# Kernel tuning notes

Measured on AMD Instinct MI355X. Metric: run time of the kernel, lower is better.

Reference implementation:

```python
import jax, jax.numpy as jnp
import numpy as np

B, IN_SIZE, IN_DIM = 16, 2048, 512
HEADS, OUT_SIZE = 4, 64
EPS = 0.1
MAX_ITER = 30
SIGMA = 0.1


def setup_inputs() -> dict:
    key = jax.random.key(0)
    k1, k2 = jax.random.split(key)
    x = jax.random.normal(k1, (B, IN_SIZE, IN_DIM), dtype=jnp.float32)
    stdv = 1.0 / np.sqrt(OUT_SIZE)
    weight = jax.random.uniform(k2, (HEADS, OUT_SIZE, IN_DIM), jnp.float32, -stdv, stdv)
    return {"x": x, "weight": weight}


def _position_filter(in_size, out_size, sigma):
    # 1-D gaussian position filter (image=False branch of get_position_filter)
    a = jnp.arange(0.0, in_size, dtype=jnp.float32)[:, None] / in_size
    b = jnp.arange(0.0, out_size, dtype=jnp.float32)[None, :] / out_size
    return jnp.exp(-(((a - b) / sigma) ** 2))  # (in_size, out_size)


def log_sinkhorn(K, iterations):
    """Log-domain Sinkhorn. K: (B, H, N, M) log-kernel.
    Row marginal a = 1/N (uniform, no mask). Scaling vectors are
    detached (envelope trick) before forming the transport plan,
    matching the original OTK implementation."""
    Bn, H, N, M = K.shape
    log_a = jnp.full((Bn, H, N), -jnp.log(jnp.float32(N)), dtype=K.dtype)
    u0 = jnp.zeros((Bn, H, N), K.dtype)
    v0 = jnp.zeros((Bn, H, M), K.dtype)

    def step(carry, _):
        u, v = carry
        Z = K + u[..., :, None] + v[..., None, :]
        u = log_a - jax.nn.logsumexp(Z, axis=-1)
        Z = K + u[..., :, None] + v[..., None, :]
        v = -jax.nn.logsumexp(Z, axis=-2)
        return (u, v), None

    (u, v), _ = jax.lax.scan(step, (u0, v0), None, length=iterations)
    u = jax.lax.stop_gradient(u)
    v = jax.lax.stop_gradient(v)
    return jnp.exp(K + u[..., :, None] + v[..., None, :])  # (B,H,N,M)


def reference(x, weight):
    # x: (B, N, D); weight: (H, M, D)
    pf = _position_filter(IN_SIZE, OUT_SIZE, SIGMA)  # (N, M)
    # euclidean cost via expansion (cdist)
    x2 = jnp.sum(x * x, axis=-1)                      # (B, N)
    w2 = jnp.sum(weight * weight, axis=-1)            # (H, M)
    xw = jnp.einsum('bnd,hmd->bhnm', x, weight)       # (B, H, N, M)
    C = jnp.sqrt(jnp.maximum(x2[:, None, :, None] + w2[None, :, None, :] - 2.0 * xw, 0.0))
    K = (-C / EPS) * pf[None, None]                   # position filter applied to log-kernel
    P = log_sinkhorn(K, MAX_ITER)                     # (B, H, N, M) transport plan
    # attn: (B, M, H, N) -> (B, M*H, N)
    attn = jnp.transpose(P, (0, 3, 1, 2)).reshape(B, OUT_SIZE * HEADS, IN_SIZE)
    out = jnp.matmul(attn, x)                         # (B, M*H, D)
    return out.reshape(B, OUT_SIZE, HEADS * IN_DIM)
```

## Files before the change

kernel.cpp:

```cpp
#include <hip/hip_runtime.h>
#include <hip/hip_fp16.h>


typedef _Float16 h2 __attribute__((ext_vector_type(2)));
typedef _Float16 h8 __attribute__((ext_vector_type(8)));
typedef float f4 __attribute__((ext_vector_type(4)));

#define NB 16
#define NN 2048
#define ND 512
#define NH 4
#define NM 64
#define NITER 30
#define EUSCALE 8.0f

static __device__ __forceinline__ float fdot2f(h2 a, h2 b, float c) {
#if __has_builtin(__builtin_amdgcn_fdot2)
  return __builtin_amdgcn_fdot2(a, b, c, false);
#else
  return (float)a[0] * (float)b[0] + (float)a[1] * (float)b[1] + c;
#endif
}

static __device__ __forceinline__ h2 pkrtz(float a, float b) {
  return __builtin_bit_cast(h2, __builtin_amdgcn_cvt_pkrtz(a, b));
}

static __device__ __forceinline__ h8 pack8(float4 a, float4 b) {
  h8 r;
  r[0] = (_Float16)a.x; r[1] = (_Float16)a.y; r[2] = (_Float16)a.z; r[3] = (_Float16)a.w;
  r[4] = (_Float16)b.x; r[5] = (_Float16)b.y; r[6] = (_Float16)b.z; r[7] = (_Float16)b.w;
  return r;
}

static __device__ __forceinline__ float sq4(float4 a) {
  return a.x * a.x + a.y * a.y + a.z * a.z + a.w * a.w;
}

__global__ __launch_bounds__(512) void k01_fused(const float* __restrict__ x,
                                                 const float* __restrict__ w,
                                                 _Float16* __restrict__ xT,
                                                 _Float16* __restrict__ E) {
  extern __shared__ __align__(16) char smem[];
  const int bid = blockIdx.x;
  const int tid = threadIdx.x;

  if (bid < 2048) {
    auto tile = (float(*)[65])smem;
    const int sub = tid >> 8;
    const int t = tid & 255;
    const int xt = bid & 15;
    const int dt = (bid >> 4) & 7;
    const int b = bid >> 7;
    const int n0 = (xt * 2 + sub) * 64;
    const int d0 = dt * 64;
    const int rbase = sub << 6;

    const int nr = t >> 2;
    const int ds = (t & 3) * 16;
    const float4* src = (const float4*)(x + ((size_t)(b * NN + n0 + nr) * ND + d0 + ds));
    float4 v0 = src[0], v1 = src[1], v2 = src[2], v3 = src[3];
    float vals[16] = {v0.x, v0.y, v0.z, v0.w, v1.x, v1.y, v1.z, v1.w,
                      v2.x, v2.y, v2.z, v2.w, v3.x, v3.y, v3.z, v3.w};
#pragma unroll
    for (int j = 0; j < 16; ++j) tile[rbase + ds + j][nr] = vals[j];
    __syncthreads();
    const int dr = t >> 2;
    const int ns = (t & 3) * 16;
    h8 o0, o1;
#pragma unroll
    for (int j = 0; j < 8; ++j) o0[j] = (_Float16)tile[rbase + dr][ns + j];
#pragma unroll
    for (int j = 0; j < 8; ++j) o1[j] = (_Float16)tile[rbase + dr][ns + 8 + j];
    _Float16* dst = xT + ((size_t)(b * ND + d0 + dr) * NN + n0 + ns);
    *(h8*)dst = o0;
    *(h8*)(dst + 8) = o1;
    return;
  }

  auto Ah  = (_Float16(*)[72])(smem);
  auto Bh  = (_Float16(*)[72])(smem + 18432);
  auto x2s = (float(*)[4])(smem + 55296);
  auto w2s = (float(*)[2])(smem + 57344);
  float* x2r = (float*)(smem + 59392);
  float* w2r = (float*)(smem + 59904);

  const int bid2 = bid - 2048;
  const int b = bid2 >> 4;
  const int n0 = (bid2 & 15) * 128;
  const int lane = tid & 63;
  const int wv = tid >> 6;
  const int lrow = lane & 15;
  const int kq = lane >> 4;

  f4 acc[16];
#pragma unroll
  for (int i = 0; i < 16; ++i) acc[i] = (f4){0.f, 0.f, 0.f, 0.f};

  const int ar = tid >> 2, ac = (tid & 3) * 16;
  const int br = tid >> 1, bc = (tid & 1) * 32;
  const float* xsrc = x + ((size_t)(b * NN + n0 + ar) * ND + ac);
  const float* wsrc = w + ((size_t)br * ND + bc);
  float x2p = 0.f, w2p = 0.f;

  for (int kt = 0; kt < 8; ++kt) {
    {
      const float4* s4 = (const float4*)(xsrc + kt * 64);
      float4 a0 = s4[0], a1 = s4[1], a2 = s4[2], a3 = s4[3];
      x2p += sq4(a0) + sq4(a1) + sq4(a2) + sq4(a3);
      *(h8*)&Ah[ar][ac] = pack8(a0, a1);
      *(h8*)&Ah[ar][ac + 8] = pack8(a2, a3);
    }
    {
      const float4* s4 = (const float4*)(wsrc + kt * 64);
      float4 u0 = s4[0], u1 = s4[1], u2 = s4[2], u3 = s4[3];
      float4 u4 = s4[4], u5 = s4[5], u6 = s4[6], u7 = s4[7];
      w2p += sq4(u0) + sq4(u1) + sq4(u2) + sq4(u3)
           + sq4(u4) + sq4(u5) + sq4(u6) + sq4(u7);
      *(h8*)&Bh[br][bc] = pack8(u0, u1);
      *(h8*)&Bh[br][bc + 8] = pack8(u2, u3);
      *(h8*)&Bh[br][bc + 16] = pack8(u4, u5);
      *(h8*)&Bh[br][bc + 24] = pack8(u6, u7);
    }
    __syncthreads();
#pragma unroll
    for (int s = 0; s < 2; ++s) {
      h8 af = *(const h8*)&Ah[wv * 16 + lrow][s * 32 + kq * 8];
#pragma unroll
      for (int cf = 0; cf < 16; ++cf) {
        h8 bf = *(const h8*)&Bh[cf * 16 + lrow][s * 32 + kq * 8];
        acc[cf] = __builtin_amdgcn_mfma_f32_16x16x32_f16(af, bf, acc[cf], 0, 0, 0);
      }
    }
    __syncthreads();
  }

  x2s[ar][tid & 3] = x2p;
  w2s[br][tid & 1] = w2p;
  __syncthreads();
  if (tid < 128) {
    x2r[tid] = x2s[tid][0] + x2s[tid][1] + x2s[tid][2] + x2s[tid][3];
  } else if (tid < 384) {
    const int r = tid - 128;
    w2r[r] = w2s[r][0] + w2s[r][1];
  }
  __syncthreads();

#pragma unroll
  for (int cf = 0; cf < 16; ++cf) {
    const int mg = cf * 16 + lrow;
    const int hh = mg >> 6;
    const int m = mg & 63;
    const float w2v = w2r[mg];
    const float bm = (float)m * (1.0f / 64.0f);
    _Float16* Eb = E + ((size_t)(b * NH + hh) * NN) * NM;
#pragma unroll
    for (int j = 0; j < 4; ++j) {
      const int nl = wv * 16 + kq * 4 + j;
      const int n = n0 + nl;
      const float c2 = x2r[nl] + w2v - 2.0f * acc[cf][j];
      const float Cd = sqrtf(fmaxf(c2, 0.0f));
      const float tt = (float)n * (1.0f / 2048.0f) - bm;
      const float pf = __expf(-100.0f * tt * tt);
      const float Ev = __expf(-10.0f * Cd * pf);
      Eb[(size_t)n * NM + m] = (_Float16)Ev;
    }
  }
}

__global__ __launch_bounds__(512)
__attribute__((amdgpu_waves_per_eu(2, 2)))
void k2_sinkhorn(const _Float16* __restrict__ E,
                 _Float16* __restrict__ Pt) {
  const int bh = blockIdx.x;
  const int b = bh >> 2, h = bh & 3;
  const int tid = threadIdx.x;
  const int lane = tid & 63;

  __shared__ float evf[64];
  __shared__ __align__(16) h2 evh[32];
  __shared__ unsigned int pbuf[512];

  const _Float16* Ep = E + (size_t)bh * (NN * NM);

  h2 e[4][32];
#pragma unroll
  for (int i = 0; i < 4; ++i) {
    const uint4* src = (const uint4*)(Ep + (size_t)(4 * tid + i) * NM);
#pragma unroll
    for (int q = 0; q < 8; ++q) {
      uint4 v = src[q];
      e[i][q * 4 + 0] = __builtin_bit_cast(h2, v.x);
      e[i][q * 4 + 1] = __builtin_bit_cast(h2, v.y);
      e[i][q * 4 + 2] = __builtin_bit_cast(h2, v.z);
      e[i][q * 4 + 3] = __builtin_bit_cast(h2, v.w);
    }
  }

  float eu[4] = {1.f, 1.f, 1.f, 1.f};
  if (tid < 64) evf[tid] = 1.f;
  if (tid < 32) evh[tid] = pkrtz(1.f, 1.f);
  __syncthreads();

#pragma unroll 1
  for (int it = 0; it < NITER; ++it) {
    h2 evr[32];
    {
      const uint4* ev4 = (const uint4*)evh;
#pragma unroll
      for (int q8 = 0; q8 < 8; ++q8) {
        uint4 v = ev4[q8];
        evr[q8 * 4 + 0] = __builtin_bit_cast(h2, v.x);
        evr[q8 * 4 + 1] = __builtin_bit_cast(h2, v.y);
        evr[q8 * 4 + 2] = __builtin_bit_cast(h2, v.z);
        evr[q8 * 4 + 3] = __builtin_bit_cast(h2, v.w);
      }
    }
    float sa[4] = {0.f, 0.f, 0.f, 0.f};
    float sb[4] = {0.f, 0.f, 0.f, 0.f};
#pragma unroll
    for (int q = 0; q < 16; ++q) {
#pragma unroll
      for (int i = 0; i < 4; ++i) sa[i] = fdot2f(e[i][q], evr[q], sa[i]);
    }
#pragma unroll
    for (int q = 16; q < 32; ++q) {
#pragma unroll
      for (int i = 0; i < 4; ++i) sb[i] = fdot2f(e[i][q], evr[q], sb[i]);
    }
#pragma unroll
    for (int i = 0; i < 4; ++i) {
      eu[i] = 4.8828125e-4f * __builtin_amdgcn_rcpf(eu[i] * (sa[i] + sb[i]));
    }
    h2 eup[4];
#pragma unroll
    for (int i = 0; i < 4; ++i) {
      const float es = eu[i] * EUSCALE;
      eup[i] = pkrtz(es, es);
    }
    h2 tp[32];
#pragma unroll
    for (int q = 0; q < 32; ++q) {
      tp[q] = e[0][q] * eup[0] + e[1][q] * eup[1];
      tp[q] += e[2][q] * eup[2] + e[3][q] * eup[3];
    }
#pragma unroll
    for (int k = 0; k < 5; ++k) {
      const int nn = 32 >> k;
      const bool up = (lane >> k) & 1;
#pragma unroll
      for (int p = 0; p < (nn >> 1); ++p) {
        h2 keep = up ? tp[p + (nn >> 1)] : tp[p];
        h2 send = up ? tp[p] : tp[p + (nn >> 1)];
        int rv = __shfl_xor(__builtin_bit_cast(int, send), 1 << k, 64);
        tp[p] = keep + __builtin_bit_cast(h2, rv);
      }
    }
    pbuf[tid] = __builtin_bit_cast(unsigned int, tp[0]);
    __syncthreads();
    if (tid < 32) {
      const int j = tid;
      const int rev = ((j & 1) << 4) | ((j & 2) << 2) | (j & 4) | ((j & 8) >> 2) | ((j & 16) >> 4);
      float T0 = 0.f, T1 = 0.f;
#pragma unroll
      for (int wq = 0; wq < 8; ++wq) {
        h2 a = __builtin_bit_cast(h2, pbuf[wq * 64 + rev]);
        h2 c = __builtin_bit_cast(h2, pbuf[wq * 64 + rev + 32]);
        T0 += (float)a[0] + (float)c[0];
        T1 += (float)a[1] + (float)c[1];
      }
      const float e0 = evf[2 * j], e1 = evf[2 * j + 1];
      const float n0 = EUSCALE * __builtin_amdgcn_rcpf(e0 * T0);
      const float n1 = EUSCALE * __builtin_amdgcn_rcpf(e1 * T1);
      evf[2 * j] = n0;
      evf[2 * j + 1] = n1;
      evh[j] = pkrtz(n0, n1);
    }
    __syncthreads();
  }

  _Float16* Pb = Pt + ((size_t)(b * 256 + h)) * NN;
#pragma unroll
  for (int q = 0; q < 32; ++q) {
    const float ev0 = evf[2 * q];
    const float ev1 = evf[2 * q + 1];
    float a0[4], a1[4];
#pragma unroll
    for (int i = 0; i < 4; ++i) {
      a0[i] = (float)e[i][q][0] * eu[i] * ev0;
      a1[i] = (float)e[i][q][1] * eu[i] * ev1;
    }
    uint2 st0, st1;
    st0.x = __builtin_bit_cast(unsigned int, pkrtz(a0[0], a0[1]));
    st0.y = __builtin_bit_cast(unsigned int, pkrtz(a0[2], a0[3]));
    st1.x = __builtin_bit_cast(unsigned int, pkrtz(a1[0], a1[1]));
    st1.y = __builtin_bit_cast(unsigned int, pkrtz(a1[2], a1[3]));
    *(uint2*)(Pb + (size_t)(2 * q) * 4 * NN + 4 * tid) = st0;
    *(uint2*)(Pb + (size_t)(2 * q + 1) * 4 * NN + 4 * tid) = st1;
  }
}

__global__ __launch_bounds__(256) void k3_out(const _Float16* __restrict__ Pt,
                                              const _Float16* __restrict__ xT,
                                              float* __restrict__ out) {
  __shared__ _Float16 As[64][72];
  __shared__ _Float16 Bs[64][72];
  const int b = blockIdx.z;
  const int hf = blockIdx.y;
  const int dt = blockIdx.x;
  const int tid = threadIdx.x;
  const int lane = tid & 63;
  const int wv = tid >> 6;
  const int lrow = lane & 15;
  const int kq = lane >> 4;

  f4 acc[4];
#pragma unroll
  for (int i = 0; i < 4; ++i) acc[i] = (f4){0.f, 0.f, 0.f, 0.f};

  const int ar = tid >> 2, ac = (tid & 3) * 16;
  const _Float16* asrc = Pt + ((size_t)(b * 256 + hf * 64 + ar) * NN + ac);
  const _Float16* bsrc = xT + ((size_t)(b * ND + dt * 64 + ar) * NN + ac);

  h8 a0 = *(const h8*)(asrc);
  h8 a1 = *(const h8*)(asrc + 8);
  h8 b0 = *(const h8*)(bsrc);
  h8 b1 = *(const h8*)(bsrc + 8);

  for (int kt = 0; kt < 32; ++kt) {
    *(h8*)&As[ar][ac] = a0;
    *(h8*)&As[ar][ac + 8] = a1;
    *(h8*)&Bs[ar][ac] = b0;
    *(h8*)&Bs[ar][ac + 8] = b1;
    __syncthreads();
    if (kt < 31) {
      const int k0 = (kt + 1) * 64;
      a0 = *(const h8*)(asrc + k0);
      a1 = *(const h8*)(asrc + k0 + 8);
      b0 = *(const h8*)(bsrc + k0);
      b1 = *(const h8*)(bsrc + k0 + 8);
    }
#pragma unroll
    for (int s = 0; s < 2; ++s) {
      h8 af = *(const h8*)&As[wv * 16 + lrow][s * 32 + kq * 8];
#pragma unroll
      for (int cf = 0; cf < 4; ++cf) {
        h8 bf = *(const h8*)&Bs[cf * 16 + lrow][s * 32 + kq * 8];
        acc[cf] = __builtin_amdgcn_mfma_f32_16x16x32_f16(af, bf, acc[cf], 0, 0, 0);
      }
    }
    __syncthreads();
  }
#pragma unroll
  for (int cf = 0; cf < 4; ++cf) {
    const int d = dt * 64 + cf * 16 + lrow;
#pragma unroll
    for (int j = 0; j < 4; ++j) {
      const int row = hf * 64 + wv * 16 + kq * 4 + j;
      out[(size_t)(b * 256 + row) * ND + d] = acc[cf][j];
    }
  }
}

extern "C" void kernel_launch(void* const* d_in, const int* in_sizes, int n_in,
                              void* d_out, int out_size, void* d_ws, size_t ws_size,
                              hipStream_t stream) {
  const float* x = (const float*)d_in[0];
  const float* w = (const float*)d_in[1];
  float* out = (float*)d_out;
  char* ws = (char*)d_ws;
  _Float16* xT = (_Float16*)ws;
  _Float16* E  = (_Float16*)(ws + (size_t)33554432);
  _Float16* Pt = (_Float16*)(ws + (size_t)50331648);

  k01_fused<<<2304, 512, 60928, stream>>>(x, w, xT, E);
  k2_sinkhorn<<<64, 512, 0, stream>>>(E, Pt);
  k3_out<<<dim3(8, 4, NB), 256, 0, stream>>>(Pt, xT, out);
}
```

Baseline: 161.8 us.

## Overlap x transpose with Sinkhorn and stage half of E in LDS

The x-to-fp16 transpose moves out of the E-building kernel and into the Sinkhorn launch as extra blocks, so the transpose runs alongside the 64 long Sinkhorn blocks on otherwise idle CUs. The Sinkhorn blocks no longer hold all of E in registers. Half is kept in XOR-swizzled LDS (128KB of dynamic shared memory) and the other half is re-read from global (L2) every iteration. This frees registers, but adds LDS and global traffic inside each iteration and drops the waves-per-eu hint.

```diff
diff --git a/kernel.cpp b/kernel.cpp
--- a/kernel.cpp
+++ b/kernel.cpp
@@ -37,57 +37,19 @@
   return a.x * a.x + a.y * a.y + a.z * a.z + a.w * a.w;
 }
 
-__global__ __launch_bounds__(512) void k01_fused(const float* __restrict__ x,
+__global__ __launch_bounds__(512) void k1_buildE(const float* __restrict__ x,
                                                  const float* __restrict__ w,
-                                                 _Float16* __restrict__ xT,
                                                  _Float16* __restrict__ E) {
-  extern __shared__ __align__(16) char smem[];
-  const int bid = blockIdx.x;
+  __shared__ _Float16 Ah[128][72];
+  __shared__ _Float16 Bh[256][72];
+  __shared__ float x2s[128][4];
+  __shared__ float w2s[256][2];
+  __shared__ float x2r[128];
+  __shared__ float w2r[256];
+
+  const int b = blockIdx.y;
+  const int n0 = blockIdx.x * 128;
   const int tid = threadIdx.x;
-
-  if (bid < 2048) {
-    auto tile = (float(*)[65])smem;
-    const int sub = tid >> 8;
-    const int t = tid & 255;
-    const int xt = bid & 15;
-    const int dt = (bid >> 4) & 7;
-    const int b = bid >> 7;
-    const int n0 = (xt * 2 + sub) * 64;
-    const int d0 = dt * 64;
-    const int rbase = sub << 6;
-
-    const int nr = t >> 2;
-    const int ds = (t & 3) * 16;
-    const float4* src = (const float4*)(x + ((size_t)(b * NN + n0 + nr) * ND + d0 + ds));
-    float4 v0 = src[0], v1 = src[1], v2 = src[2], v3 = src[3];
-    float vals[16] = {v0.x, v0.y, v0.z, v0.w, v1.x, v1.y, v1.z, v1.w,
-                      v2.x, v2.y, v2.z, v2.w, v3.x, v3.y, v3.z, v3.w};
-#pragma unroll
-    for (int j = 0; j < 16; ++j) tile[rbase + ds + j][nr] = vals[j];
-    __syncthreads();
-    const int dr = t >> 2;
-    const int ns = (t & 3) * 16;
-    h8 o0, o1;
-#pragma unroll
-    for (int j = 0; j < 8; ++j) o0[j] = (_Float16)tile[rbase + dr][ns + j];
-#pragma unroll
-    for (int j = 0; j < 8; ++j) o1[j] = (_Float16)tile[rbase + dr][ns + 8 + j];
-    _Float16* dst = xT + ((size_t)(b * ND + d0 + dr) * NN + n0 + ns);
-    *(h8*)dst = o0;
-    *(h8*)(dst + 8) = o1;
-    return;
-  }
-
-  auto Ah  = (_Float16(*)[72])(smem);
-  auto Bh  = (_Float16(*)[72])(smem + 18432);
-  auto x2s = (float(*)[4])(smem + 55296);
-  auto w2s = (float(*)[2])(smem + 57344);
-  float* x2r = (float*)(smem + 59392);
-  float* w2r = (float*)(smem + 59904);
-
-  const int bid2 = bid - 2048;
-  const int b = bid2 >> 4;
-  const int n0 = (bid2 & 15) * 128;
   const int lane = tid & 63;
   const int wv = tid >> 6;
   const int lrow = lane & 15;
@@ -168,33 +130,69 @@
   }
 }
 
-__global__ __launch_bounds__(512)
-__attribute__((amdgpu_waves_per_eu(2, 2)))
-void k2_sinkhorn(const _Float16* __restrict__ E,
-                 _Float16* __restrict__ Pt) {
-  const int bh = blockIdx.x;
+__global__ __launch_bounds__(512) void k20_fused(const float* __restrict__ x,
+                                                 const _Float16* __restrict__ E,
+                                                 _Float16* __restrict__ xT,
+                                                 _Float16* __restrict__ Pt) {
+  extern __shared__ __align__(16) char smem[];
+  const int bid = blockIdx.x;
+  const int tid = threadIdx.x;
+
+  if (bid >= 64) {
+    auto tile = (float(*)[65])smem;
+    const int sub = tid >> 8;
+    const int t = tid & 255;
+    const int bid2 = bid - 64;
+#pragma unroll
+    for (int p = 0; p < 2; ++p) {
+      if (p) __syncthreads();
+      const int t4 = bid2 * 4 + p * 2 + sub;
+      const int b = t4 >> 8;
+      const int rem = t4 & 255;
+      const int n0 = (rem & 31) * 64;
+      const int d0 = (rem >> 5) * 64;
+      const int rbase = sub << 6;
+      const int nr = t >> 2;
+      const int ds = (t & 3) * 16;
+      const float4* src = (const float4*)(x + ((size_t)(b * NN + n0 + nr) * ND + d0 + ds));
+      float4 v0 = src[0], v1 = src[1], v2 = src[2], v3 = src[3];
+      float vals[16] = {v0.x, v0.y, v0.z, v0.w, v1.x, v1.y, v1.z, v1.w,
+                        v2.x, v2.y, v2.z, v2.w, v3.x, v3.y, v3.z, v3.w};
+#pragma unroll
+      for (int j = 0; j < 16; ++j) tile[rbase + ds + j][nr] = vals[j];
+      __syncthreads();
+      const int dr = t >> 2;
+      const int ns = (t & 3) * 16;
+      h8 o0, o1;
+#pragma unroll
+      for (int j = 0; j < 8; ++j) o0[j] = (_Float16)tile[rbase + dr][ns + j];
+#pragma unroll
+      for (int j = 0; j < 8; ++j) o1[j] = (_Float16)tile[rbase + dr][ns + 8 + j];
+      _Float16* dst = xT + ((size_t)(b * ND + d0 + dr) * NN + n0 + ns);
+      *(h8*)dst = o0;
+      *(h8*)(dst + 8) = o1;
+    }
+    return;
+  }
+
+  const int bh = bid;
   const int b = bh >> 2, h = bh & 3;
-  const int tid = threadIdx.x;
   const int lane = tid & 63;
 
-  __shared__ float evf[64];
-  __shared__ __align__(16) h2 evh[32];
-  __shared__ unsigned int pbuf[512];
+  uint4* Ech = (uint4*)smem;
+  float* evf = (float*)(smem + 131072);
+  h2* evh = (h2*)(smem + 131328);
+  unsigned int* pbuf = (unsigned int*)(smem + 131456);
 
   const _Float16* Ep = E + (size_t)bh * (NN * NM);
-
-  h2 e[4][32];
-#pragma unroll
-  for (int i = 0; i < 4; ++i) {
+  const int sw = tid & 7;
+
+#pragma unroll
+  for (int i = 0; i < 2; ++i) {
     const uint4* src = (const uint4*)(Ep + (size_t)(4 * tid + i) * NM);
-#pragma unroll
-    for (int q = 0; q < 8; ++q) {
-      uint4 v = src[q];
-      e[i][q * 4 + 0] = __builtin_bit_cast(h2, v.x);
-      e[i][q * 4 + 1] = __builtin_bit_cast(h2, v.y);
-      e[i][q * 4 + 2] = __builtin_bit_cast(h2, v.z);
-      e[i][q * 4 + 3] = __builtin_bit_cast(h2, v.w);
-    }
+    uint4* dst = Ech + (size_t)(2 * tid + i) * 8;
+#pragma unroll
+    for (int j = 0; j < 8; ++j) dst[j ^ sw] = src[j];
   }
 
   float eu[4] = {1.f, 1.f, 1.f, 1.f};
@@ -204,6 +202,7 @@
 
 #pragma unroll 1
   for (int it = 0; it < NITER; ++it) {
+    asm volatile("" ::: "memory");
     h2 evr[32];
     {
       const uint4* ev4 = (const uint4*)evh;
@@ -216,6 +215,31 @@
         evr[q8 * 4 + 3] = __builtin_bit_cast(h2, v.w);
       }
     }
+    h2 e[4][32];
+#pragma unroll
+    for (int i = 0; i < 2; ++i) {
+      const uint4* slot = Ech + (size_t)(2 * tid + i) * 8;
+#pragma unroll
+      for (int j = 0; j < 8; ++j) {
+        uint4 v = slot[j ^ sw];
+        e[i][j * 4 + 0] = __builtin_bit_cast(h2, v.x);
+        e[i][j * 4 + 1] = __builtin_bit_cast(h2, v.y);
+        e[i][j * 4 + 2] = __builtin_bit_cast(h2, v.z);
+        e[i][j * 4 + 3] = __builtin_bit_cast(h2, v.w);
+      }
+    }
+#pragma unroll
+    for (int i = 2; i < 4; ++i) {
+      const uint4* src = (const uint4*)(Ep + (size_t)(4 * tid + i) * NM);
+#pragma unroll
+      for (int j = 0; j < 8; ++j) {
+        uint4 v = src[j];
+        e[i][j * 4 + 0] = __builtin_bit_cast(h2, v.x);
+        e[i][j * 4 + 1] = __builtin_bit_cast(h2, v.y);
+        e[i][j * 4 + 2] = __builtin_bit_cast(h2, v.z);
+        e[i][j * 4 + 3] = __builtin_bit_cast(h2, v.w);
+      }
+    }
     float sa[4] = {0.f, 0.f, 0.f, 0.f};
     float sb[4] = {0.f, 0.f, 0.f, 0.f};
 #pragma unroll
@@ -279,6 +303,32 @@
     __syncthreads();
   }
 
+  asm volatile("" ::: "memory");
+  h2 ee[4][32];
+#pragma unroll
+  for (int i = 0; i < 2; ++i) {
+    const uint4* slot = Ech + (size_t)(2 * tid + i) * 8;
+#pragma unroll
+    for (int j = 0; j < 8; ++j) {
+      uint4 v = slot[j ^ sw];
+      ee[i][j * 4 + 0] = __builtin_bit_cast(h2, v.x);
+      ee[i][j * 4 + 1] = __builtin_bit_cast(h2, v.y);
+      ee[i][j * 4 + 2] = __builtin_bit_cast(h2, v.z);
+      ee[i][j * 4 + 3] = __builtin_bit_cast(h2, v.w);
+    }
+  }
+#pragma unroll
+  for (int i = 2; i < 4; ++i) {
+    const uint4* src = (const uint4*)(Ep + (size_t)(4 * tid + i) * NM);
+#pragma unroll
+    for (int j = 0; j < 8; ++j) {
+      uint4 v = src[j];
+      ee[i][j * 4 + 0] = __builtin_bit_cast(h2, v.x);
+      ee[i][j * 4 + 1] = __builtin_bit_cast(h2, v.y);
+      ee[i][j * 4 + 2] = __builtin_bit_cast(h2, v.z);
+      ee[i][j * 4 + 3] = __builtin_bit_cast(h2, v.w);
+    }
+  }
   _Float16* Pb = Pt + ((size_t)(b * 256 + h)) * NN;
 #pragma unroll
   for (int q = 0; q < 32; ++q) {
@@ -287,8 +337,8 @@
     float a0[4], a1[4];
 #pragma unroll
     for (int i = 0; i < 4; ++i) {
-      a0[i] = (float)e[i][q][0] * eu[i] * ev0;
-      a1[i] = (float)e[i][q][1] * eu[i] * ev1;
+      a0[i] = (float)ee[i][q][0] * eu[i] * ev0;
+      a1[i] = (float)ee[i][q][1] * eu[i] * ev1;
     }
     uint2 st0, st1;
     st0.x = __builtin_bit_cast(unsigned int, pkrtz(a0[0], a0[1]));
@@ -373,7 +423,10 @@
   _Float16* E  = (_Float16*)(ws + (size_t)33554432);
   _Float16* Pt = (_Float16*)(ws + (size_t)50331648);
 
-  k01_fused<<<2304, 512, 60928, stream>>>(x, w, xT, E);
-  k2_sinkhorn<<<64, 512, 0, stream>>>(E, Pt);
+  (void)hipFuncSetAttribute((const void*)k20_fused,
+                            hipFuncAttributeMaxDynamicSharedMemorySize, 135168);
+
+  k1_buildE<<<dim3(16, NB), 512, 0, stream>>>(x, w, E);
+  k20_fused<<<64 + 1024, 512, 133504, stream>>>(x, E, xT, Pt);
   k3_out<<<dim3(8, 4, NB), 256, 0, stream>>>(Pt, xT, out);
 }
```

Result: slower. 256.0 us (+58.2%).

## Move x transpose into the Sinkhorn launch to overlap with it

Applied to the files above, without the earlier changes.

The fp16 transpose of x (xT) moves out of the E-building kernel and into the Sinkhorn kernel as 1024 extra blocks, each handling two 64x64 tiles. The aim is to fill idle CUs during the 64-block Sinkhorn phase with transpose work, and to shrink the first kernel so it only computes E. The two block types share a union of shared memory, which makes the shared allocation larger for the Sinkhorn blocks. Whether this helps depends on the Sinkhorn blocks getting scheduled early alongside the transpose blocks.

```diff
diff --git a/kernel.cpp b/kernel.cpp
--- a/kernel.cpp
+++ b/kernel.cpp
@@ -37,57 +37,19 @@
   return a.x * a.x + a.y * a.y + a.z * a.z + a.w * a.w;
 }
 
-__global__ __launch_bounds__(512) void k01_fused(const float* __restrict__ x,
+__global__ __launch_bounds__(512) void k1_buildE(const float* __restrict__ x,
                                                  const float* __restrict__ w,
-                                                 _Float16* __restrict__ xT,
                                                  _Float16* __restrict__ E) {
-  extern __shared__ __align__(16) char smem[];
-  const int bid = blockIdx.x;
+  __shared__ _Float16 Ah[128][72];
+  __shared__ _Float16 Bh[256][72];
+  __shared__ float x2s[128][4];
+  __shared__ float w2s[256][2];
+  __shared__ float x2r[128];
+  __shared__ float w2r[256];
+
+  const int b = blockIdx.y;
+  const int n0 = blockIdx.x * 128;
   const int tid = threadIdx.x;
-
-  if (bid < 2048) {
-    auto tile = (float(*)[65])smem;
-    const int sub = tid >> 8;
-    const int t = tid & 255;
-    const int xt = bid & 15;
-    const int dt = (bid >> 4) & 7;
-    const int b = bid >> 7;
-    const int n0 = (xt * 2 + sub) * 64;
-    const int d0 = dt * 64;
-    const int rbase = sub << 6;
-
-    const int nr = t >> 2;
-    const int ds = (t & 3) * 16;
-    const float4* src = (const float4*)(x + ((size_t)(b * NN + n0 + nr) * ND + d0 + ds));
-    float4 v0 = src[0], v1 = src[1], v2 = src[2], v3 = src[3];
-    float vals[16] = {v0.x, v0.y, v0.z, v0.w, v1.x, v1.y, v1.z, v1.w,
-                      v2.x, v2.y, v2.z, v2.w, v3.x, v3.y, v3.z, v3.w};
-#pragma unroll
-    for (int j = 0; j < 16; ++j) tile[rbase + ds + j][nr] = vals[j];
-    __syncthreads();
-    const int dr = t >> 2;
-    const int ns = (t & 3) * 16;
-    h8 o0, o1;
-#pragma unroll
-    for (int j = 0; j < 8; ++j) o0[j] = (_Float16)tile[rbase + dr][ns + j];
-#pragma unroll
-    for (int j = 0; j < 8; ++j) o1[j] = (_Float16)tile[rbase + dr][ns + 8 + j];
-    _Float16* dst = xT + ((size_t)(b * ND + d0 + dr) * NN + n0 + ns);
-    *(h8*)dst = o0;
-    *(h8*)(dst + 8) = o1;
-    return;
-  }
-
-  auto Ah  = (_Float16(*)[72])(smem);
-  auto Bh  = (_Float16(*)[72])(smem + 18432);
-  auto x2s = (float(*)[4])(smem + 55296);
-  auto w2s = (float(*)[2])(smem + 57344);
-  float* x2r = (float*)(smem + 59392);
-  float* w2r = (float*)(smem + 59904);
-
-  const int bid2 = bid - 2048;
-  const int b = bid2 >> 4;
-  const int n0 = (bid2 & 15) * 128;
   const int lane = tid & 63;
   const int wv = tid >> 6;
   const int lrow = lane & 15;
@@ -168,18 +130,65 @@
   }
 }
 
-__global__ __launch_bounds__(512)
-__attribute__((amdgpu_waves_per_eu(2, 2)))
-void k2_sinkhorn(const _Float16* __restrict__ E,
-                 _Float16* __restrict__ Pt) {
-  const int bh = blockIdx.x;
+__global__ __launch_bounds__(512) void k20_fused(const float* __restrict__ x,
+                                                 const _Float16* __restrict__ E,
+                                                 _Float16* __restrict__ xT,
+                                                 _Float16* __restrict__ Pt) {
+  __shared__ union {
+    float tile[128][65];
+    struct {
+      float evf[64];
+      h2 evh[32];
+      unsigned int pbuf[512];
+    } s2;
+  } sm;
+  const int bid = blockIdx.x;
+  const int tid = threadIdx.x;
+
+  if (bid >= 64) {
+    auto tile = sm.tile;
+    const int sub = tid >> 8;
+    const int t = tid & 255;
+    const int bid2 = bid - 64;
+#pragma unroll
+    for (int p = 0; p < 2; ++p) {
+      if (p) __syncthreads();
+      const int t4 = bid2 * 4 + p * 2 + sub;
+      const int b = t4 >> 8;
+      const int rem = t4 & 255;
+      const int n0 = (rem & 31) * 64;
+      const int d0 = (rem >> 5) * 64;
+      const int rbase = sub << 6;
+      const int nr = t >> 2;
+      const int ds = (t & 3) * 16;
+      const float4* src = (const float4*)(x + ((size_t)(b * NN + n0 + nr) * ND + d0 + ds));
+      float4 v0 = src[0], v1 = src[1], v2 = src[2], v3 = src[3];
+      float vals[16] = {v0.x, v0.y, v0.z, v0.w, v1.x, v1.y, v1.z, v1.w,
+                        v2.x, v2.y, v2.z, v2.w, v3.x, v3.y, v3.z, v3.w};
+#pragma unroll
+      for (int j = 0; j < 16; ++j) tile[rbase + ds + j][nr] = vals[j];
+      __syncthreads();
+      const int dr = t >> 2;
+      const int ns = (t & 3) * 16;
+      h8 o0, o1;
+#pragma unroll
+      for (int j = 0; j < 8; ++j) o0[j] = (_Float16)tile[rbase + dr][ns + j];
+#pragma unroll
+      for (int j = 0; j < 8; ++j) o1[j] = (_Float16)tile[rbase + dr][ns + 8 + j];
+      _Float16* dst = xT + ((size_t)(b * ND + d0 + dr) * NN + n0 + ns);
+      *(h8*)dst = o0;
+      *(h8*)(dst + 8) = o1;
+    }
+    return;
+  }
+
+  const int bh = bid;
   const int b = bh >> 2, h = bh & 3;
-  const int tid = threadIdx.x;
   const int lane = tid & 63;
 
-  __shared__ float evf[64];
-  __shared__ __align__(16) h2 evh[32];
-  __shared__ unsigned int pbuf[512];
+  float* evf = sm.s2.evf;
+  h2* evh = sm.s2.evh;
+  unsigned int* pbuf = sm.s2.pbuf;
 
   const _Float16* Ep = E + (size_t)bh * (NN * NM);
 
@@ -373,7 +382,7 @@
   _Float16* E  = (_Float16*)(ws + (size_t)33554432);
   _Float16* Pt = (_Float16*)(ws + (size_t)50331648);
 
-  k01_fused<<<2304, 512, 60928, stream>>>(x, w, xT, E);
-  k2_sinkhorn<<<64, 512, 0, stream>>>(E, Pt);
+  k1_buildE<<<dim3(16, NB), 512, 0, stream>>>(x, w, E);
+  k20_fused<<<64 + 1024, 512, 0, stream>>>(x, E, xT, Pt);
   k3_out<<<dim3(8, 4, NB), 256, 0, stream>>>(Pt, xT, out);
 }
```

Measured after the change: 151.3 us (median of 2 runs). 1.07x faster.
